# Kernel optimization log

Hardware: AMD Instinct MI355X
Metric: run time of the kernel (lower is better)

Reference implementation:

```python
import jax, jax.numpy as jnp
import numpy as np

B, H, W, C, HID, V, EMB = 16, 24, 96, 1024, 256, 5000, 256
BN_EPS = 1e-5


def _lin(k, fin, fout, s=0.05):
    return jax.random.normal(k, (fin, fout), jnp.float32) * s


def setup_inputs():
    ks = jax.random.split(jax.random.key(0), 24)
    inp = {
        "input_y": jax.random.randint(ks[0], (B,), 0, V),
        "input_hidden": jax.random.normal(ks[1], (B, 1, HID), jnp.float32),
        "img_feature": jax.random.normal(ks[2], (B, C, H, W), jnp.float32),
        "feature_w": W,
        "attention_sum": jnp.zeros((B, 1, H, W), jnp.float32),
        "alpha_t": jax.random.uniform(ks[3], (B, 1, H, W), jnp.float32),
        "feature_h": H,
        "batch_size": B,
        "h_mask": jax.random.randint(ks[4], (B,), 1, H + 1),
        "w_mask": jax.random.randint(ks[5], (B,), 1, W + 1),
        "emb_table": jax.random.normal(ks[6], (V, EMB), jnp.float32) * 0.05,
        "gru1_wi": _lin(ks[7], EMB, 3 * HID), "gru1_wh": _lin(ks[8], HID, 3 * HID),
        "gru1_bi": jnp.zeros((3 * HID,), jnp.float32), "gru1_bh": jnp.zeros((3 * HID,), jnp.float32),
        "fc1_w": _lin(ks[9], HID, 256), "fc1_b": jnp.zeros((256,), jnp.float32),
        "gru2_wi": _lin(ks[10], C, 3 * HID), "gru2_wh": _lin(ks[11], HID, 3 * HID),
        "gru2_bi": jnp.zeros((3 * HID,), jnp.float32), "gru2_bh": jnp.zeros((3 * HID,), jnp.float32),
        "out_w": _lin(ks[12], 128, V), "out_b": jnp.zeros((V,), jnp.float32),
        "emb2_w": _lin(ks[13], 256, 128), "emb2_b": jnp.zeros((128,), jnp.float32),
        "conv1_w": jax.random.normal(ks[14], (1, 1, 3, 3), jnp.float32) * 0.05,
        "conv1_b": jnp.zeros((1,), jnp.float32),
        "conv_tan_w": jax.random.normal(ks[15], (256, 256, 3, 3), jnp.float32) * 0.02,
        "conv_tan_b": jnp.zeros((256,), jnp.float32),
        "fc2_w": _lin(ks[16], HID, 128), "fc2_b": jnp.zeros((128,), jnp.float32),
        "ua_w": _lin(ks[17], C, 256), "ua_b": jnp.zeros((256,), jnp.float32),
        "uf_w": _lin(ks[18], 1, 256), "uf_b": jnp.zeros((256,), jnp.float32),
        "v_w": _lin(ks[19], 256, 1), "v_b": jnp.zeros((1,), jnp.float32),
        "wc_w": _lin(ks[20], C, 128), "wc_b": jnp.zeros((128,), jnp.float32),
        "bn1_gamma": jnp.ones((256,), jnp.float32), "bn1_beta": jnp.zeros((256,), jnp.float32),
        "bn1_mean": jnp.zeros((256,), jnp.float32), "bn1_var": jnp.ones((256,), jnp.float32),
    }
    return inp


def _gru(x, h, wi, wh, bi, bh):
    # PyTorch GRUCell semantics
    gi = x @ wi + bi
    gh = h @ wh + bh
    ir, iz, inn = jnp.split(gi, 3, axis=-1)
    hr, hz, hn = jnp.split(gh, 3, axis=-1)
    r = jax.nn.sigmoid(ir + hr)
    z = jax.nn.sigmoid(iz + hz)
    n = jnp.tanh(inn + r * hn)
    return (1.0 - z) * n + z * h


def _conv(x, w, b):
    y = jax.lax.conv_general_dilated(x, w, (1, 1), 'SAME',
                                     dimension_numbers=('NCHW', 'OIHW', 'NCHW'))
    return y + b[None, :, None, None]


def reference(input_y, input_hidden, img_feature, feature_w, attention_sum, alpha_t,
              feature_h, batch_size, h_mask, w_mask,
              emb_table, gru1_wi, gru1_wh, gru1_bi, gru1_bh, fc1_w, fc1_b,
              gru2_wi, gru2_wh, gru2_bi, gru2_bh, out_w, out_b, emb2_w, emb2_b,
              conv1_w, conv1_b, conv_tan_w, conv_tan_b, fc2_w, fc2_b,
              ua_w, ua_b, uf_w, uf_b, v_w, v_b, wc_w, wc_b,
              bn1_gamma, bn1_beta, bn1_mean, bn1_var):
    b, c, h, w = img_feature.shape
    # per-sample validity mask over the feature map  [B, H, W]
    et_mask = ((jnp.arange(h)[None, :] < h_mask[:, None])[:, :, None]
               & (jnp.arange(w)[None, :] < w_mask[:, None])[:, None, :]).astype(jnp.float32)

    emb = emb_table[input_y]                      # [B, 256] (dropout = identity, eval)
    h0 = input_hidden[:, 0, :]                    # [B, HID]
    st1 = _gru(emb, h0, gru1_wi, gru1_wh, gru1_bi, gru1_bh)
    st1 = st1 @ fc1_w + fc1_b                     # [B, 256]

    alpha_c = _conv(alpha_t, conv1_w, conv1_b)    # [B, 1, H, W]
    att_sum = attention_sum + alpha_c             # coverage accumulator

    img1 = jnp.einsum('bchw,cd->bhwd', img_feature, ua_w) + ua_b  # [B,H,W,256]
    att1 = att_sum[:, 0, :, :, None] * uf_w[0] + uf_b             # Linear(1,256)
    et = st1[:, None, None, :] + img1 + att1      # [B, H, W, 256]

    et_nchw = jnp.transpose(et, (0, 3, 1, 2))
    et_nchw = _conv(et_nchw, conv_tan_w, conv_tan_b)
    et_nchw = et_nchw * et_mask[:, None]
    inv = bn1_gamma / jnp.sqrt(bn1_var + BN_EPS)  # eval-mode BatchNorm2d(256)
    et_nchw = (et_nchw - bn1_mean[None, :, None, None]) * inv[None, :, None, None] \
              + bn1_beta[None, :, None, None]
    et_nchw = jnp.tanh(et_nchw)

    e = jnp.einsum('bchw,c->bhw', et_nchw, v_w[:, 0]) + v_b[0]    # [B, H, W]
    e_exp = jnp.exp(e) * et_mask
    e_sum = jnp.sum(e_exp, axis=(1, 2))
    alpha = e_exp / (e_sum[:, None, None] + 1e-8)                 # masked softmax

    ct = jnp.einsum('bhw,bchw->bc', alpha, img_feature)           # [B, 1024]
    st = _gru(ct, st1, gru2_wi, gru2_wh, gru2_bi, gru2_bh)        # [B, HID]
    hidden_next = st[:, None, :]

    pre = (st @ fc2_w + fc2_b) + (emb @ emb2_w + emb2_b) + (ct @ wc_w + wc_b)  # [B,128]
    output = jax.nn.log_softmax(pre @ out_w + out_b, axis=1)[:, None, :]       # [B,1,V]
    return output, hidden_next, alpha[:, None], att_sum
```

## Files before the change

kernel.cpp:

```cpp
#include <hip/hip_runtime.h>
#include <hip/hip_bf16.h>

#define B   16
#define H   24
#define W   96
#define C   1024
#define HID 256
#define V   5000
#define EMB 256
#define HW  (H*W)
#define BN_EPS 1e-5f
#define H2  (H+2)
#define W2  (W+2)

#define OUT0 0
#define OUT1 (B*V)
#define OUT2 (OUT1 + B*HID)
#define OUT3 (OUT2 + B*HW)

#define WSB_IMGT  0
#define WSB_ETP   75497472
#define WSB_WTB   96370688
#define WSB_UAT   97550336
#define WSB_E     98074624
#define WSB_ST1   98369536
#define WSB_CT    98385920
#define WSB_PRE   98451456
#define WSB_GIGH1 98459648
#define WSB_GH2   98574336
#define WSB_GI2   98631680

typedef __attribute__((ext_vector_type(8))) short short8;
typedef __attribute__((ext_vector_type(4))) float f32x4;

__device__ inline unsigned short f2bf(float f) {
    union { float f; unsigned int u; } v; v.f = f;
    unsigned int r = v.u + 0x7fffu + ((v.u >> 16) & 1u);
    return (unsigned short)(r >> 16);
}
__device__ inline float bf2f(unsigned short u) {
    union { unsigned int u; float f; } v; v.u = ((unsigned int)u) << 16;
    return v.f;
}

__global__ __launch_bounds__(256) void k_imgT(const float* img, unsigned short* imgT)
{
    int hw0 = blockIdx.x*128, c1 = blockIdx.y*128, b = blockIdx.z;
    int t = threadIdx.x;
    __shared__ unsigned short tr[128*136];
    #pragma unroll
    for (int i = 0; i < 16; ++i) {
        int flat = i*1024 + t*4;
        int r = flat >> 7;
        int col = flat & 127;
        float4 v = *(const float4*)&img[((size_t)(b*C + c1 + r))*HW + hw0 + col];
        tr[(col+0)*136 + r] = f2bf(v.x);
        tr[(col+1)*136 + r] = f2bf(v.y);
        tr[(col+2)*136 + r] = f2bf(v.z);
        tr[(col+3)*136 + r] = f2bf(v.w);
    }
    __syncthreads();
    #pragma unroll
    for (int i = 0; i < 8; ++i) {
        int flat = i*2048 + t*8;
        int orow = flat >> 7;
        int oc = flat & 127;
        *(short8*)&imgT[((size_t)(b*HW) + hw0 + orow)*1024 + c1 + oc] =
            *(const short8*)&tr[orow*136 + oc];
    }
}

__global__ __launch_bounds__(256) void k_prep(
    const float* conv_w_src, unsigned short* wtb,
    const float* ua_w, unsigned short* uat,
    const float* att_in, const float* alpha_t, const float* cw, const float* cb, float* att_out,
    float* ct, unsigned short* et_p)
{
    int x = blockIdx.x, t = threadIdx.x;
    if (x < 2304) {
        int idx = x*256 + t;
        int c = idx & 255; int o = (idx >> 8) & 255; int khw = idx >> 16;
        wtb[(khw*256 + o)*256 + c] = f2bf(conv_w_src[(o*256 + c)*9 + khw]);
    } else if (x < 3328) {
        int idx = (x - 2304)*256 + t;
        int c = idx & 1023; int d = idx >> 10;
        uat[d*1024 + c] = f2bf(ua_w[c*256 + d]);
    } else if (x < 3472) {
        int i = (x - 3328)*256 + t;
        int w = i % W; int h = (i / W) % H; int b = i / HW;
        float s = cb[0];
        #pragma unroll
        for (int kh = 0; kh < 3; ++kh) {
            int r = h + kh - 1; if (r < 0 || r >= H) continue;
            #pragma unroll
            for (int kw = 0; kw < 3; ++kw) {
                int c = w + kw - 1; if (c < 0 || c >= W) continue;
                s += alpha_t[(b*H + r)*W + c]*cw[kh*3+kw];
            }
        }
        att_out[i] = att_in[i] + s;
    } else if (x < 3536) {
        ct[(x - 3472)*256 + t] = 0.f;
    } else {
        int flat = (x - 3536)*256 + t;
        int b = flat / 7808; int r = flat - b*7808;
        int h2, w2, j;
        if (r < 3136)      { h2 = 0;  w2 = r >> 5;          j = r & 31; }
        else if (r < 6272) { h2 = 25; w2 = (r - 3136) >> 5; j = (r - 3136) & 31; }
        else {
            int rr = r - 6272;
            h2 = 1 + (rr >> 6);
            int s = rr & 63;
            w2 = (s < 32) ? 0 : 97;
            j = s & 31;
        }
        ((int4*)et_p)[((size_t)(b*H2 + h2)*W2 + w2)*32 + j] = make_int4(0,0,0,0);
    }
}

__global__ __launch_bounds__(256) void k_tail1(
    const int* y, const float* emb_table, const float* h0,
    const float* wi, const float* wh, float* gigh)
{
    int virt = blockIdx.x*16;
    int t = threadIdx.x;
    bool gi_mode = virt < 768;
    __shared__ float a_l[16*256];
    for (int i = t; i < 4096; i += 256) {
        int b = i >> 8, k = i & 255;
        a_l[i] = gi_mode ? emb_table[y[b]*EMB + k] : h0[b*HID + k];
    }
    __syncthreads();
    int nl = t & 15, b = t >> 4;
    int n = (gi_mode ? virt : virt - 768) + nl;
    const float* wp = gi_mode ? wi : wh;
    float acc = 0.f;
    #pragma unroll 16
    for (int k = 0; k < 256; ++k) acc += a_l[b*256 + k]*wp[k*768 + n];
    gigh[b*1536 + virt + nl] = acc;
}

__global__ __launch_bounds__(256) void k_fc1c(
    const float* gigh, const float* h0, const float* bi, const float* bh,
    const float* fc1_w, const float* fc1_b, float* st1)
{
    int n0 = blockIdx.x*16, t = threadIdx.x;
    __shared__ float a_l[16*256];
    for (int i = t; i < 4096; i += 256) {
        int b = i >> 8, k = i & 255;
        const float* g = gigh + b*1536;
        float ir = g[k] + bi[k], iz = g[256+k] + bi[256+k], in_ = g[512+k] + bi[512+k];
        float hr = g[768+k] + bh[k], hz = g[1024+k] + bh[256+k], hn = g[1280+k] + bh[512+k];
        float r = 1.f/(1.f+__expf(-(ir+hr)));
        float z = 1.f/(1.f+__expf(-(iz+hz)));
        float n = tanhf(in_ + r*hn);
        a_l[i] = (1.f - z)*n + z*h0[b*HID + k];
    }
    __syncthreads();
    int nl = t & 15, b = t >> 4;
    float acc = fc1_b[n0+nl];
    #pragma unroll 16
    for (int k = 0; k < 256; ++k) acc += a_l[b*256+k]*fc1_w[k*256 + n0 + nl];
    st1[b*256 + n0 + nl] = acc;
}

__global__ __launch_bounds__(256, 3) void k_et(
    const unsigned short* imgT, const unsigned short* uat, const float* ua_b,
    const float* st1, const float* att_sum, const float* uf_w, const float* uf_b,
    unsigned short* et_p)
{
    int h = blockIdx.x, ny = blockIdx.y, b = blockIdx.z;
    int t = threadIdx.x;
    int wv = t >> 6, lane = t & 63, q = lane >> 4, ln = lane & 15;
    int n0 = ny*128 + wv*32;
    __shared__ __align__(16) unsigned short a_l[96*136];

    f32x4 acc[12];
    #pragma unroll
    for (int i = 0; i < 12; ++i) acc[i] = (f32x4){0.f,0.f,0.f,0.f};

    const unsigned short* ab = imgT + ((size_t)(b*HW) + h*W)*1024;
    const unsigned short* bbase = uat + (size_t)(n0 + ln)*1024 + q*8;

    for (int c0 = 0; c0 < 1024; c0 += 128) {
        __syncthreads();
        #pragma unroll
        for (int i = t; i < 1536; i += 256) {
            int m = i >> 4, j = i & 15;
            ((int4*)a_l)[m*17 + j] = *((const int4*)(ab + (size_t)m*1024 + c0) + j);
        }
        __syncthreads();
        #pragma unroll
        for (int cs = 0; cs < 128; cs += 32) {
            short8 av[6];
            #pragma unroll
            for (int mf = 0; mf < 6; ++mf)
                av[mf] = *(const short8*)&a_l[(ln + 16*mf)*136 + cs + q*8];
            #pragma unroll
            for (int j = 0; j < 2; ++j) {
                short8 bv = *(const short8*)(bbase + (size_t)(j*16)*1024 + c0 + cs);
                #pragma unroll
                for (int mf = 0; mf < 6; ++mf)
                    acc[mf*2+j] = __builtin_amdgcn_mfma_f32_16x16x32_bf16(av[mf], bv, acc[mf*2+j], 0, 0, 0);
            }
        }
    }

    float att_m[24];
    #pragma unroll
    for (int mf = 0; mf < 6; ++mf)
        #pragma unroll
        for (int r = 0; r < 4; ++r)
            att_m[mf*4+r] = att_sum[(b*H + h)*W + mf*16 + q*4 + r];
    #pragma unroll
    for (int j = 0; j < 2; ++j) {
        int n = n0 + j*16 + ln;
        float s1 = st1[b*256 + n] + ua_b[n];
        float ufw = uf_w[n], ufb = uf_b[n];
        #pragma unroll
        for (int mf = 0; mf < 6; ++mf)
            #pragma unroll
            for (int r = 0; r < 4; ++r) {
                int m = mf*16 + q*4 + r;
                float v = acc[mf*2+j][r] + s1 + att_m[mf*4+r]*ufw + ufb;
                et_p[((size_t)(b*H2 + h + 1)*W2 + (m + 1))*256 + n] = f2bf(v);
            }
    }
}

__global__ __launch_bounds__(256, 3) void k_conv(
    const unsigned short* et_p, const unsigned short* wtb, const float* cb,
    const float* bn_g, const float* bn_b, const float* bn_m, const float* bn_v,
    const float* v_w, float* e_part)
{
    int h = blockIdx.x, ny = blockIdx.y, b = blockIdx.z;
    int t = threadIdx.x;
    int wv = t >> 6, lane = t & 63, q = lane >> 4, ln = lane & 15;
    int n0 = ny*128 + wv*32;
    __shared__ __align__(16) unsigned short patch[3*98*72];
    __shared__ float lds_red[4][96];

    f32x4 acc[12];
    #pragma unroll
    for (int i = 0; i < 12; ++i) acc[i] = (f32x4){0.f,0.f,0.f,0.f};

    for (int c0 = 0; c0 < 256; c0 += 64) {
        __syncthreads();
        for (int i = t; i < 2352; i += 256) {
            int kh = i / 784; int r = i - kh*784; int x = r >> 3; int j = r & 7;
            const int4* src = (const int4*)et_p + ((size_t)(b*H2 + h + kh)*W2 + x)*32 + (c0 >> 3) + j;
            ((int4*)patch)[kh*882 + x*9 + j] = *src;
        }
        __syncthreads();
        #pragma unroll
        for (int kh = 0; kh < 3; ++kh) {
            #pragma unroll
            for (int kw = 0; kw < 3; ++kw) {
                const unsigned short* brow = wtb + ((size_t)((kh*3 + kw)*256 + n0 + ln))*256 + c0 + q*8;
                #pragma unroll
                for (int cs = 0; cs < 64; cs += 32) {
                    short8 av[6];
                    #pragma unroll
                    for (int mf = 0; mf < 6; ++mf)
                        av[mf] = *(const short8*)&patch[kh*7056 + (ln + 16*mf + kw)*72 + cs + q*8];
                    #pragma unroll
                    for (int j = 0; j < 2; ++j) {
                        short8 bv = *(const short8*)(brow + j*4096 + cs);
                        #pragma unroll
                        for (int mf = 0; mf < 6; ++mf)
                            acc[mf*2+j] = __builtin_amdgcn_mfma_f32_16x16x32_bf16(av[mf], bv, acc[mf*2+j], 0, 0, 0);
                    }
                }
            }
        }
    }

    float psum[24];
    #pragma unroll
    for (int i = 0; i < 24; ++i) psum[i] = 0.f;
    #pragma unroll
    for (int j = 0; j < 2; ++j) {
        int o = n0 + j*16 + ln;
        float inv  = bn_g[o]*rsqrtf(bn_v[o] + BN_EPS);
        float mean = bn_m[o], beta = bn_b[o], bias = cb[o], vw = v_w[o];
        #pragma unroll
        for (int mf = 0; mf < 6; ++mf)
            #pragma unroll
            for (int r = 0; r < 4; ++r) {
                float x = (acc[mf*2+j][r] + bias - mean)*inv + beta;
                x = fminf(fmaxf(x, -15.f), 15.f);
                float ex = __expf(2.f*x);
                psum[mf*4+r] += ((ex - 1.f)/(ex + 1.f))*vw;
            }
    }
    #pragma unroll
    for (int s = 1; s < 16; s <<= 1)
        #pragma unroll
        for (int i = 0; i < 24; ++i) psum[i] += __shfl_xor(psum[i], s);
    if (ln == 0) {
        #pragma unroll
        for (int mf = 0; mf < 6; ++mf)
            #pragma unroll
            for (int r = 0; r < 4; ++r)
                lds_red[wv][mf*16 + q*4 + r] = psum[mf*4+r];
    }
    __syncthreads();
    if (t < 96)
        e_part[(size_t)ny*(B*HW) + (b*H + h)*W + t] =
            lds_red[0][t] + lds_red[1][t] + lds_red[2][t] + lds_red[3][t];
}

__global__ __launch_bounds__(256) void k_softmax(
    const float* e_part, const int* h_mask, const int* w_mask, const float* v_b,
    float* alpha_out)
{
    int b = blockIdx.x, t = threadIdx.x;
    int hm = h_mask[b], wm = w_mask[b];
    float vb = v_b[0];
    __shared__ float red[256];
    float vals[9];
    float loc = 0.f;
    #pragma unroll
    for (int i = 0; i < 9; ++i) {
        int hw = t + i*256;
        int hh = hw / W, ww = hw % W;
        float v = 0.f;
        if (hh < hm && ww < wm)
            v = __expf(e_part[b*HW + hw] + e_part[B*HW + b*HW + hw] + vb);
        vals[i] = v; loc += v;
    }
    red[t] = loc; __syncthreads();
    for (int s = 128; s > 0; s >>= 1) { if (t < s) red[t] += red[t+s]; __syncthreads(); }
    float inv = 1.f/(red[0] + 1e-8f);
    #pragma unroll
    for (int i = 0; i < 9; ++i) alpha_out[b*HW + t + i*256] = vals[i]*inv;
}

__global__ __launch_bounds__(256) void k_ct(
    const float* alpha, const unsigned short* imgT, float* ct)
{
    int s = blockIdx.x, b = blockIdx.y, t = threadIdx.x;
    int cg = (t & 127)*8, half = t >> 7;
    float acc[8];
    #pragma unroll
    for (int j = 0; j < 8; ++j) acc[j] = 0.f;
    for (int i = 0; i < 96; ++i) {
        int hw = s*192 + i*2 + half;
        float a = alpha[b*HW + hw];
        union { short8 v; unsigned short u[8]; } pk;
        pk.v = *(const short8*)&imgT[((size_t)(b*HW) + hw)*1024 + cg];
        #pragma unroll
        for (int j = 0; j < 8; ++j) acc[j] += a*bf2f(pk.u[j]);
    }
    #pragma unroll
    for (int j = 0; j < 8; ++j) atomicAdd(&ct[b*1024 + cg + j], acc[j]);
}

__global__ __launch_bounds__(256) void k_g2(
    const float* st1, const int* y, const float* emb_table,
    const float* wh, const float* emb2_w, float* gh2,
    const float* ct, const float* wi, const float* wc_w, float* gi2p)
{
    int x = blockIdx.x, t = threadIdx.x;
    __shared__ float a_l[16*256];
    if (x < 56) {
        int virt = x*16;
        bool ghm = virt < 768;
        for (int i = t; i < 4096; i += 256) {
            int b = i >> 8, k = i & 255;
            a_l[i] = ghm ? st1[b*256 + k] : emb_table[y[b]*EMB + k];
        }
        __syncthreads();
        int nl = t & 15, b = t >> 4;
        float acc = 0.f;
        if (ghm) {
            int n = virt + nl;
            #pragma unroll 16
            for (int k = 0; k < 256; ++k) acc += a_l[b*256+k]*wh[k*768 + n];
        } else {
            int n = virt - 768 + nl;
            #pragma unroll 16
            for (int k = 0; k < 256; ++k) acc += a_l[b*256+k]*emb2_w[k*128 + n];
        }
        gh2[b*896 + virt + nl] = acc;
    } else {
        int xx = x - 56;
        int ks = xx / 56, virt = (xx - ks*56)*16;
        int k0 = ks*256;
        for (int i = t; i < 4096; i += 256) {
            int b = i >> 8, k = i & 255;
            a_l[i] = ct[b*1024 + k0 + k];
        }
        __syncthreads();
        int nl = t & 15, b = t >> 4;
        float acc = 0.f;
        if (virt < 768) {
            int n = virt + nl;
            #pragma unroll 16
            for (int k = 0; k < 256; ++k) acc += a_l[b*256+k]*wi[(k0+k)*768 + n];
        } else {
            int n = virt - 768 + nl;
            #pragma unroll 16
            for (int k = 0; k < 256; ++k) acc += a_l[b*256+k]*wc_w[(k0+k)*128 + n];
        }
        gi2p[(ks*16 + b)*896 + virt + nl] = acc;
    }
}

__global__ __launch_bounds__(256) void k_fc2c(
    const float* gi2p, const float* gh2, const float* st1,
    const float* bi, const float* bh,
    const float* fc2_w, const float* fc2_b, const float* emb2_b, const float* wc_b,
    float* hidden_out, float* pre)
{
    int n0 = blockIdx.x*16, t = threadIdx.x;
    __shared__ float st_l[16*256];
    for (int i = t; i < 4096; i += 256) {
        int b = i >> 8, k = i & 255;
        float ir = bi[k], iz = bi[256+k], in_ = bi[512+k];
        #pragma unroll
        for (int ks = 0; ks < 4; ++ks) {
            const float* g = gi2p + (ks*16 + b)*896;
            ir += g[k]; iz += g[256+k]; in_ += g[512+k];
        }
        const float* gh = gh2 + b*896;
        float hr = gh[k] + bh[k], hz = gh[256+k] + bh[256+k], hn = gh[512+k] + bh[512+k];
        float h = st1[b*256+k];
        float r = 1.f/(1.f+__expf(-(ir+hr)));
        float z = 1.f/(1.f+__expf(-(iz+hz)));
        float n = tanhf(in_ + r*hn);
        float s = (1.f - z)*n + z*h;
        st_l[i] = s;
        if (blockIdx.x == 0) hidden_out[b*HID + k] = s;
    }
    __syncthreads();
    int nl = t & 15, b = t >> 4;
    int n = n0 + nl;
    float acc = fc2_b[n] + emb2_b[n] + wc_b[n] + gh2[b*896 + 768 + n];
    #pragma unroll
    for (int ks = 0; ks < 4; ++ks) acc += gi2p[(ks*16 + b)*896 + 768 + n];
    #pragma unroll 16
    for (int k = 0; k < 256; ++k) acc += st_l[b*256+k]*fc2_w[k*128 + n];
    pre[b*128 + n] = acc;
}

__global__ __launch_bounds__(256) void k_logits(
    const float* pre, const float* out_w, const float* out_b, float* out)
{
    int j0 = blockIdx.x*64, t = threadIdx.x;
    __shared__ float pre_l[16*128];
    for (int i = t; i < 2048; i += 256) pre_l[i] = pre[i];
    __syncthreads();
    int jl = t & 63, bg = t >> 6;
    int j = j0 + jl;
    if (j >= V) return;
    float acc0=0.f, acc1=0.f, acc2=0.f, acc3=0.f;
    const float* pl = pre_l + bg*4*128;
    #pragma unroll 8
    for (int k = 0; k < 128; ++k) {
        float wv = out_w[k*V + j];
        acc0 += pl[k]*wv; acc1 += pl[128+k]*wv; acc2 += pl[256+k]*wv; acc3 += pl[384+k]*wv;
    }
    float ob = out_b[j];
    out[(bg*4+0)*V + j] = acc0 + ob;
    out[(bg*4+1)*V + j] = acc1 + ob;
    out[(bg*4+2)*V + j] = acc2 + ob;
    out[(bg*4+3)*V + j] = acc3 + ob;
}

__global__ __launch_bounds__(1024) void k_lsm(float* out)
{
    int b = blockIdx.x, t = threadIdx.x;
    __shared__ float red[1024];
    float lg[5]; float mx = -1e30f;
    #pragma unroll
    for (int i = 0; i < 5; ++i) {
        int j = t + i*1024;
        lg[i] = (j < V) ? out[b*V + j] : -1e30f;
        mx = fmaxf(mx, lg[i]);
    }
    red[t] = mx; __syncthreads();
    for (int s = 512; s > 0; s >>= 1) { if (t < s) red[t] = fmaxf(red[t], red[t+s]); __syncthreads(); }
    float gmax = red[0]; __syncthreads();
    float se = 0.f;
    #pragma unroll
    for (int i = 0; i < 5; ++i) { int j = t + i*1024; if (j < V) se += __expf(lg[i] - gmax); }
    red[t] = se; __syncthreads();
    for (int s = 512; s > 0; s >>= 1) { if (t < s) red[t] += red[t+s]; __syncthreads(); }
    float lse = logf(red[0]);
    #pragma unroll
    for (int i = 0; i < 5; ++i) { int j = t + i*1024; if (j < V) out[b*V + j] = lg[i] - gmax - lse; }
}

extern "C" void kernel_launch(void* const* d_in, const int* in_sizes, int n_in,
                              void* d_out, int out_size, void* d_ws, size_t ws_size,
                              hipStream_t stream)
{
    const int*   input_y      = (const int*)  d_in[0];
    const float* input_hidden = (const float*)d_in[1];
    const float* img          = (const float*)d_in[2];
    const float* attention    = (const float*)d_in[4];
    const float* alpha_t      = (const float*)d_in[5];
    const int*   h_mask       = (const int*)  d_in[8];
    const int*   w_mask       = (const int*)  d_in[9];
    const float* emb_table    = (const float*)d_in[10];
    const float* gru1_wi      = (const float*)d_in[11];
    const float* gru1_wh      = (const float*)d_in[12];
    const float* gru1_bi      = (const float*)d_in[13];
    const float* gru1_bh      = (const float*)d_in[14];
    const float* fc1_w        = (const float*)d_in[15];
    const float* fc1_b        = (const float*)d_in[16];
    const float* gru2_wi      = (const float*)d_in[17];
    const float* gru2_wh      = (const float*)d_in[18];
    const float* gru2_bi      = (const float*)d_in[19];
    const float* gru2_bh      = (const float*)d_in[20];
    const float* out_w        = (const float*)d_in[21];
    const float* out_b        = (const float*)d_in[22];
    const float* emb2_w       = (const float*)d_in[23];
    const float* emb2_b       = (const float*)d_in[24];
    const float* conv1_w      = (const float*)d_in[25];
    const float* conv1_b      = (const float*)d_in[26];
    const float* conv_tan_w   = (const float*)d_in[27];
    const float* conv_tan_b   = (const float*)d_in[28];
    const float* fc2_w        = (const float*)d_in[29];
    const float* fc2_b        = (const float*)d_in[30];
    const float* ua_w         = (const float*)d_in[31];
    const float* ua_b         = (const float*)d_in[32];
    const float* uf_w         = (const float*)d_in[33];
    const float* uf_b         = (const float*)d_in[34];
    const float* v_w          = (const float*)d_in[35];
    const float* v_b          = (const float*)d_in[36];
    const float* wc_w         = (const float*)d_in[37];
    const float* wc_b         = (const float*)d_in[38];
    const float* bn1_gamma    = (const float*)d_in[39];
    const float* bn1_beta     = (const float*)d_in[40];
    const float* bn1_mean     = (const float*)d_in[41];
    const float* bn1_var      = (const float*)d_in[42];

    float* out = (float*)d_out;
    char*  ws  = (char*)d_ws;
    unsigned short* imgT = (unsigned short*)(ws + WSB_IMGT);
    unsigned short* et_p = (unsigned short*)(ws + WSB_ETP);
    unsigned short* wtb  = (unsigned short*)(ws + WSB_WTB);
    unsigned short* uat  = (unsigned short*)(ws + WSB_UAT);
    float* e_part = (float*)(ws + WSB_E);
    float* st1   = (float*)(ws + WSB_ST1);
    float* ct    = (float*)(ws + WSB_CT);
    float* pre   = (float*)(ws + WSB_PRE);
    float* gigh1 = (float*)(ws + WSB_GIGH1);
    float* gh2   = (float*)(ws + WSB_GH2);
    float* gi2p  = (float*)(ws + WSB_GI2);

    float* out_logits = out + OUT0;
    float* out_hidden = out + OUT1;
    float* out_alpha  = out + OUT2;
    float* out_attsum = out + OUT3;

    k_imgT<<<dim3(HW/128, C/128, B), 256, 0, stream>>>(img, imgT);
    k_prep<<<4024, 256, 0, stream>>>(conv_tan_w, wtb, ua_w, uat,
                                     attention, alpha_t, conv1_w, conv1_b, out_attsum,
                                     ct, et_p);
    k_tail1<<<96, 256, 0, stream>>>(input_y, emb_table, input_hidden,
                                    gru1_wi, gru1_wh, gigh1);
    k_fc1c<<<16, 256, 0, stream>>>(gigh1, input_hidden, gru1_bi, gru1_bh,
                                   fc1_w, fc1_b, st1);
    k_et<<<dim3(H, 2, B), 256, 0, stream>>>(imgT, uat, ua_b, st1, out_attsum,
                                            uf_w, uf_b, et_p);
    k_conv<<<dim3(H, 2, B), 256, 0, stream>>>(et_p, wtb, conv_tan_b,
                                              bn1_gamma, bn1_beta, bn1_mean, bn1_var,
                                              v_w, e_part);
    k_softmax<<<B, 256, 0, stream>>>(e_part, h_mask, w_mask, v_b, out_alpha);
    k_ct<<<dim3(12, B), 256, 0, stream>>>(out_alpha, imgT, ct);
    k_g2<<<280, 256, 0, stream>>>(st1, input_y, emb_table, gru2_wh, emb2_w, gh2,
                                  ct, gru2_wi, wc_w, gi2p);
    k_fc2c<<<8, 256, 0, stream>>>(gi2p, gh2, st1, gru2_bi, gru2_bh,
                                  fc2_w, fc2_b, emb2_b, wc_b, out_hidden, pre);
    k_logits<<<(V + 63)/64, 256, 0, stream>>>(pre, out_w, out_b, out_logits);
    k_lsm<<<B, 1024, 0, stream>>>(out_logits);
}
```

Before: 549.1 us.

## Swizzle LDS layouts in transpose, et and conv kernels; resplit ct grid

Replaces the padded shared-memory layouts in the image transpose, et GEMM and conv kernels with XOR-swizzled layouts, so the MFMA operand reads and the staging writes avoid bank conflicts without padding. The transpose kernel now has each thread gather 8 channels per output row, using 64-row tiles and a grid twice as wide. The ct reduction is split into 16 spatial chunks per batch instead of 12, giving more blocks and shorter loops. The transpose now does strided scalar global reads, which may coalesce worse than the previous float4 reads.

```diff
diff --git a/kernel.cpp b/kernel.cpp
--- a/kernel.cpp
+++ b/kernel.cpp
@@ -45,28 +45,28 @@
 
 __global__ __launch_bounds__(256) void k_imgT(const float* img, unsigned short* imgT)
 {
-    int hw0 = blockIdx.x*128, c1 = blockIdx.y*128, b = blockIdx.z;
+    int hw0 = blockIdx.x*64, c0 = blockIdx.y*128, b = blockIdx.z;
     int t = threadIdx.x;
-    __shared__ unsigned short tr[128*136];
-    #pragma unroll
-    for (int i = 0; i < 16; ++i) {
-        int flat = i*1024 + t*4;
-        int r = flat >> 7;
-        int col = flat & 127;
-        float4 v = *(const float4*)&img[((size_t)(b*C + c1 + r))*HW + hw0 + col];
-        tr[(col+0)*136 + r] = f2bf(v.x);
-        tr[(col+1)*136 + r] = f2bf(v.y);
-        tr[(col+2)*136 + r] = f2bf(v.z);
-        tr[(col+3)*136 + r] = f2bf(v.w);
+    __shared__ __align__(16) unsigned short tr[64*256];
+    int row = t & 63;
+    int sgb = t >> 6;
+    const float* src = img + ((size_t)b*C + c0)*HW + hw0 + row;
+    #pragma unroll
+    for (int k = 0; k < 4; ++k) {
+        int sg = sgb + k*4;
+        union { short8 v; unsigned short u[8]; } pk;
+        #pragma unroll
+        for (int j = 0; j < 8; ++j)
+            pk.u[j] = f2bf(src[(size_t)(sg*8 + j)*HW]);
+        *(short8*)&tr[row*256 + (sg ^ (row & 31))*8] = pk.v;
     }
     __syncthreads();
     #pragma unroll
-    for (int i = 0; i < 8; ++i) {
-        int flat = i*2048 + t*8;
-        int orow = flat >> 7;
-        int oc = flat & 127;
-        *(short8*)&imgT[((size_t)(b*HW) + hw0 + orow)*1024 + c1 + oc] =
-            *(const short8*)&tr[orow*136 + oc];
+    for (int k = 0; k < 4; ++k) {
+        int i = k*256 + t;
+        int orow = i >> 4, sg = i & 15;
+        *(short8*)&imgT[((size_t)(b*HW) + hw0 + orow)*1024 + c0 + sg*8] =
+            *(const short8*)&tr[orow*256 + (sg ^ (orow & 31))*8];
     }
 }
 
@@ -173,7 +173,7 @@
     int t = threadIdx.x;
     int wv = t >> 6, lane = t & 63, q = lane >> 4, ln = lane & 15;
     int n0 = ny*128 + wv*32;
-    __shared__ __align__(16) unsigned short a_l[96*136];
+    __shared__ __align__(16) unsigned short a_l[96*256];
 
     f32x4 acc[12];
     #pragma unroll
@@ -182,12 +182,18 @@
     const unsigned short* ab = imgT + ((size_t)(b*HW) + h*W)*1024;
     const unsigned short* bbase = uat + (size_t)(n0 + ln)*1024 + q*8;
 
+    int sw8 = (q ^ ((ln & 7) << 2)) << 3;
+    int ebase[6];
+    #pragma unroll
+    for (int mf = 0; mf < 6; ++mf) ebase[mf] = (ln + 16*mf)*256 + sw8;
+
     for (int c0 = 0; c0 < 1024; c0 += 128) {
         __syncthreads();
         #pragma unroll
         for (int i = t; i < 1536; i += 256) {
-            int m = i >> 4, j = i & 15;
-            ((int4*)a_l)[m*17 + j] = *((const int4*)(ab + (size_t)m*1024 + c0) + j);
+            int m = i >> 4, sg = i & 15;
+            ((int4*)a_l)[m*32 + (sg ^ ((m & 7) << 2))] =
+                *((const int4*)(ab + (size_t)m*1024 + c0) + sg);
         }
         __syncthreads();
         #pragma unroll
@@ -195,7 +201,7 @@
             short8 av[6];
             #pragma unroll
             for (int mf = 0; mf < 6; ++mf)
-                av[mf] = *(const short8*)&a_l[(ln + 16*mf)*136 + cs + q*8];
+                av[mf] = *(const short8*)&a_l[ebase[mf] ^ cs];
             #pragma unroll
             for (int j = 0; j < 2; ++j) {
                 short8 bv = *(const short8*)(bbase + (size_t)(j*16)*1024 + c0 + cs);
@@ -237,19 +243,30 @@
     int t = threadIdx.x;
     int wv = t >> 6, lane = t & 63, q = lane >> 4, ln = lane & 15;
     int n0 = ny*128 + wv*32;
-    __shared__ __align__(16) unsigned short patch[3*98*72];
+    __shared__ __align__(16) unsigned short patch[3*6400];
     __shared__ float lds_red[4][96];
 
     f32x4 acc[12];
     #pragma unroll
     for (int i = 0; i < 12; ++i) acc[i] = (f32x4){0.f,0.f,0.f,0.f};
+
+    int abase[6][3];
+    #pragma unroll
+    for (int mf = 0; mf < 6; ++mf)
+        #pragma unroll
+        for (int kw = 0; kw < 3; ++kw) {
+            int x2 = ln + 16*mf + kw;
+            int sp0 = ((x2 & 3) << 3) | (q ^ (((x2 >> 2) & 3) << 1));
+            abase[mf][kw] = (x2 >> 2)*256 + sp0*8;
+        }
 
     for (int c0 = 0; c0 < 256; c0 += 64) {
         __syncthreads();
         for (int i = t; i < 2352; i += 256) {
-            int kh = i / 784; int r = i - kh*784; int x = r >> 3; int j = r & 7;
-            const int4* src = (const int4*)et_p + ((size_t)(b*H2 + h + kh)*W2 + x)*32 + (c0 >> 3) + j;
-            ((int4*)patch)[kh*882 + x*9 + j] = *src;
+            int kh = i / 784; int r = i - kh*784; int x2 = r >> 3; int sg = r & 7;
+            const int4* src = (const int4*)et_p + ((size_t)(b*H2 + h + kh)*W2 + x2)*32 + (c0 >> 3) + sg;
+            int sp = ((x2 & 3) << 3) | (sg ^ (((x2 >> 2) & 3) << 1));
+            ((int4*)patch)[kh*800 + (x2 >> 2)*32 + sp] = *src;
         }
         __syncthreads();
         #pragma unroll
@@ -262,7 +279,7 @@
                     short8 av[6];
                     #pragma unroll
                     for (int mf = 0; mf < 6; ++mf)
-                        av[mf] = *(const short8*)&patch[kh*7056 + (ln + 16*mf + kw)*72 + cs + q*8];
+                        av[mf] = *(const short8*)&patch[kh*6400 + (abase[mf][kw] ^ cs)];
                     #pragma unroll
                     for (int j = 0; j < 2; ++j) {
                         short8 bv = *(const short8*)(brow + j*4096 + cs);
@@ -344,8 +361,8 @@
     float acc[8];
     #pragma unroll
     for (int j = 0; j < 8; ++j) acc[j] = 0.f;
-    for (int i = 0; i < 96; ++i) {
-        int hw = s*192 + i*2 + half;
+    for (int i = 0; i < 72; ++i) {
+        int hw = s*144 + i*2 + half;
         float a = alpha[b*HW + hw];
         union { short8 v; unsigned short u[8]; } pk;
         pk.v = *(const short8*)&imgT[((size_t)(b*HW) + hw)*1024 + cg];
@@ -556,7 +573,7 @@
     float* out_alpha  = out + OUT2;
     float* out_attsum = out + OUT3;
 
-    k_imgT<<<dim3(HW/128, C/128, B), 256, 0, stream>>>(img, imgT);
+    k_imgT<<<dim3(HW/64, C/128, B), 256, 0, stream>>>(img, imgT);
     k_prep<<<4024, 256, 0, stream>>>(conv_tan_w, wtb, ua_w, uat,
                                      attention, alpha_t, conv1_w, conv1_b, out_attsum,
                                      ct, et_p);
@@ -570,7 +587,7 @@
                                               bn1_gamma, bn1_beta, bn1_mean, bn1_var,
                                               v_w, e_part);
     k_softmax<<<B, 256, 0, stream>>>(e_part, h_mask, w_mask, v_b, out_alpha);
-    k_ct<<<dim3(12, B), 256, 0, stream>>>(out_alpha, imgT, ct);
+    k_ct<<<dim3(16, B), 256, 0, stream>>>(out_alpha, imgT, ct);
     k_g2<<<280, 256, 0, stream>>>(st1, input_y, emb_table, gru2_wh, emb2_w, gh2,
                                   ct, gru2_wi, wc_w, gi2p);
     k_fc2c<<<8, 256, 0, stream>>>(gi2p, gh2, st1, gru2_bi, gru2_bh,
```

New measurement: 546.9 us. No clear change (-0.4%).
